# Performance work log

Hardware: AMD Instinct MI355X
Metric: run time of the kernel (lower is better)

Reference implementation:

```python
import jax, jax.numpy as jnp
import numpy as np

N_NODES = 50000
N_RAND_EDGES = 1_600_000
IN_FEATS = 512
HIDDEN = 256
NUM_CLASSES = 64


def setup_inputs() -> dict:
    key = jax.random.key(0)
    ks = jax.random.split(key, 6)
    src = jax.random.randint(ks[0], (N_RAND_EDGES,), 0, N_NODES, dtype=jnp.int32)
    dst = jax.random.randint(ks[1], (N_RAND_EDGES,), 0, N_NODES, dtype=jnp.int32)
    # dgl.add_self_loop(g): append (i, i) for every node
    loop = jnp.arange(N_NODES, dtype=jnp.int32)
    src = jnp.concatenate([src, loop])
    dst = jnp.concatenate([dst, loop])
    features = jax.random.normal(ks[2], (N_NODES, IN_FEATS), dtype=jnp.float32)
    W_conv = jax.random.normal(ks[3], (IN_FEATS, HIDDEN), dtype=jnp.float32) * (1.0 / np.sqrt(IN_FEATS))
    b_conv = jnp.zeros((HIDDEN,), dtype=jnp.float32)
    W2 = jax.random.normal(ks[4], (HIDDEN, NUM_CLASSES), dtype=jnp.float32) * (1.0 / np.sqrt(HIDDEN))
    b2 = jnp.zeros((NUM_CLASSES,), dtype=jnp.float32)
    return {"features": features, "W_conv": W_conv, "b_conv": b_conv,
            "W2": W2, "b2": b2, "src": src, "dst": dst}


def reference(features, W_conv, b_conv, W2, b2, src, dst):
    N = features.shape[0]
    ones = jnp.ones(src.shape[0], dtype=features.dtype)
    # symmetric ('both') normalization as in DGL GraphConv; self-loops guarantee deg >= 1
    deg_out = jax.ops.segment_sum(ones, src, num_segments=N)
    deg_in = jax.ops.segment_sum(ones, dst, num_segments=N)
    norm_src = jax.lax.rsqrt(deg_out)[:, None]  # [N, 1]
    norm_dst = jax.lax.rsqrt(deg_in)[:, None]
    # in_feats > hidden -> DGL multiplies by the weight before aggregating
    h = (features @ W_conv) * norm_src            # [N, H]
    agg = jax.ops.segment_sum(h[src], dst, num_segments=N)  # sparse SpMM: gather + scatter-add
    x = jax.nn.relu(agg * norm_dst + b_conv)      # [N, H]
    # dropout: identity in eval mode (deterministic reference)
    logits = x @ W2 + b2                          # [N, C]
    return jax.nn.log_softmax(logits, axis=1)
```

## Files before the change

### kernel.cpp

```cpp
#include <hip/hip_runtime.h>

typedef unsigned short u16;
typedef unsigned int u32;
typedef __attribute__((ext_vector_type(4))) float f32x4;
typedef __attribute__((ext_vector_type(8))) short s16x8;
typedef __attribute__((ext_vector_type(4))) unsigned short u16x4;
typedef __attribute__((ext_vector_type(8))) unsigned short u16x8;

#define IN_FEATS 512
#define HIDDEN   256
#define NCLS     64
#define NB       128
#define QBINS    12500
#define EPT      13

#define H8_CLIP  2.5f
#define H8_INV   (127.0f / H8_CLIP)
#define H8_SCALE (H8_CLIP / 127.0f)

static __device__ inline u16 f2bf(float f) {
    unsigned int u = __builtin_bit_cast(unsigned int, f);
    unsigned int r = (u + 0x7FFFu + ((u >> 16) & 1u)) >> 16;
    return (u16)r;
}
static __device__ inline float bf2f(u16 u) {
    unsigned int x = ((unsigned int)u) << 16;
    return __builtin_bit_cast(float, x);
}


__launch_bounds__(1024)
__global__ void khist(const int* __restrict__ src, const int* __restrict__ dst,
                      u32* __restrict__ P, int E, int N) {
    __shared__ int bins[QBINS];
    const int b = blockIdx.x;
    const int t = threadIdx.x;
    const int lo = (int)((long)b * E / NB);
    const int hi = (int)((long)(b + 1) * E / NB);

    int se[EPT], de[EPT];
#pragma unroll
    for (int p = 0; p < EPT; p++) {
        int e = lo + t + p * 1024;
        se[p] = 0; de[p] = 0;
        if (e < hi) { se[p] = src[e]; de[p] = dst[e]; }
    }

#pragma unroll 1
    for (int q = 0; q < 4; q++) {
        const int base = q * QBINS;
        __syncthreads();
        for (int j = t; j < QBINS; j += 1024) bins[j] = 0;
        __syncthreads();
#pragma unroll
        for (int p = 0; p < EPT; p++) {
            int e = lo + t + p * 1024;
            if (e < hi) {
                unsigned rs = (unsigned)(se[p] - base), rd = (unsigned)(de[p] - base);
                if (rs < (unsigned)QBINS) atomicAdd(&bins[rs], 1);
                if (rd < (unsigned)QBINS) atomicAdd(&bins[rd], 0x10000);
            }
        }
        for (int e = lo + t + EPT * 1024; e < hi; e += 1024) {
            int s = src[e], d = dst[e];
            unsigned rs = (unsigned)(s - base), rd = (unsigned)(d - base);
            if (rs < (unsigned)QBINS) atomicAdd(&bins[rs], 1);
            if (rd < (unsigned)QBINS) atomicAdd(&bins[rd], 0x10000);
        }
        __syncthreads();
        for (int j = t; j < QBINS; j += 1024) P[(size_t)b * 50000 + base + j] = (u32)bins[j];
    }
}

__global__ void kred(u32* __restrict__ P, int* __restrict__ deg_in,
                     float* __restrict__ ns, float* __restrict__ nd, int N) {
    int j = blockIdx.x * blockDim.x + threadIdx.x;
    if (j >= N) return;
    u32 so = 0, si = 0;
#pragma unroll 4
    for (int b = 0; b < NB; b++) {
        u32 v = P[(size_t)b * 50000 + j];
        P[(size_t)b * 50000 + j] = si;
        so += v & 0xffffu;
        si += v >> 16;
    }
    deg_in[j] = (int)si;
    ns[j] = rsqrtf((float)so);
    nd[j] = rsqrtf((float)si);
}

__launch_bounds__(256)
__global__ void kscanA(const int* __restrict__ deg, int* __restrict__ rowptr,
                       int* __restrict__ bsum, int N) {
    __shared__ int wsum[4];
    const int b = blockIdx.x, t = threadIdx.x;
    const int lane = t & 63, wave = t >> 6;
    const int j = b * 256 + t;
    int v = (j < N) ? deg[j] : 0;
    int s = v;
#pragma unroll
    for (int off = 1; off < 64; off <<= 1) {
        int u = __shfl_up(s, off);
        if (lane >= off) s += u;
    }
    if (lane == 63) wsum[wave] = s;
    __syncthreads();
    int woff = 0;
#pragma unroll
    for (int w = 0; w < 4; w++) woff += (w < wave) ? wsum[w] : 0;
    if (j < N) rowptr[j] = woff + s - v;
    if (t == 255) bsum[b] = woff + s;
}

__launch_bounds__(256)
__global__ void kscanB(int* __restrict__ rowptr, const int* __restrict__ bsum,
                       int N, int nblk, int E) {
    __shared__ int wsum[4];
    const int b = blockIdx.x, t = threadIdx.x;
    const int lane = t & 63, wave = t >> 6;
    int v = (t < b && t < nblk) ? bsum[t] : 0;
#pragma unroll
    for (int off = 32; off; off >>= 1) v += __shfl_xor(v, off);
    if (lane == 0) wsum[wave] = v;
    __syncthreads();
    int offsum = wsum[0] + wsum[1] + wsum[2] + wsum[3];
    int j = b * 256 + t;
    if (j < N) rowptr[j] += offsum;
    if (b == 0 && t == 0) rowptr[N] = E;
}

__launch_bounds__(1024)
__global__ void kscat(const int* __restrict__ src, const int* __restrict__ dst,
                      const int* __restrict__ rowptr, const u32* __restrict__ P,
                      int* __restrict__ csc, int E, int N) {
    __shared__ int cur[QBINS];
    const int b = blockIdx.x;
    const int t = threadIdx.x;
    const int lo = (int)((long)b * E / NB);
    const int hi = (int)((long)(b + 1) * E / NB);

    int se[EPT], de[EPT];
#pragma unroll
    for (int p = 0; p < EPT; p++) {
        int e = lo + t + p * 1024;
        se[p] = 0; de[p] = 0;
        if (e < hi) { se[p] = src[e]; de[p] = dst[e]; }
    }

#pragma unroll 1
    for (int q = 0; q < 4; q++) {
        const int base = q * QBINS;
        __syncthreads();
        for (int j = t; j < QBINS; j += 1024) {
            int node = base + j;
            cur[j] = (node < N) ? rowptr[node] + (int)P[(size_t)b * 50000 + node] : 0;
        }
        __syncthreads();
#pragma unroll
        for (int p = 0; p < EPT; p++) {
            int e = lo + t + p * 1024;
            if (e < hi) {
                unsigned rd = (unsigned)(de[p] - base);
                if (rd < (unsigned)QBINS) {
                    int pos = atomicAdd(&cur[rd], 1);
                    csc[pos] = se[p];
                }
            }
        }
        for (int e = lo + t + EPT * 1024; e < hi; e += 1024) {
            int d = dst[e];
            unsigned rd = (unsigned)(d - base);
            if (rd < (unsigned)QBINS) {
                int pos = atomicAdd(&cur[rd], 1);
                csc[pos] = src[e];
            }
        }
    }
}


__global__ void k_wt(const float* __restrict__ W, u16* __restrict__ Wt) {
    int i = blockIdx.x * blockDim.x + threadIdx.x;
    if (i < IN_FEATS * HIDDEN) {
        int k = i >> 8, n = i & 255;
        Wt[n * IN_FEATS + k] = f2bf(W[i]);
    }
}

__global__ void k_w2t(const float* __restrict__ W2, u16* __restrict__ W2t) {
    int i = blockIdx.x * blockDim.x + threadIdx.x;
    if (i < HIDDEN * NCLS) {
        int k = i >> 6, n = i & 63;
        W2t[n * HIDDEN + k] = f2bf(W2[i]);
    }
}


static __device__ inline s16x8 ld_frag(const u16* p) {
    u16x4 lo = *(const u16x4*)p;
    u16x4 hi = *(const u16x4*)(p + 4);
    s16x8 r;
    r[0] = (short)lo.x; r[1] = (short)lo.y; r[2] = (short)lo.z; r[3] = (short)lo.w;
    r[4] = (short)hi.x; r[5] = (short)hi.y; r[6] = (short)hi.z; r[7] = (short)hi.w;
    return r;
}

__launch_bounds__(512)
__global__ void k_gemm1(const float* __restrict__ feat, const u16* __restrict__ Wt,
                        const float* __restrict__ norm_src, signed char* __restrict__ h8, int N) {
    __shared__ __align__(16) u16 At[128][40];
    __shared__ __align__(16) u16 Bt[256][40];
    const int t = threadIdx.x;
    const int lane = t & 63;
    const int wave = t >> 6;
    const int wm = wave & 1;
    const int wn = wave >> 1;
    const int m0 = blockIdx.x * 128;
    const int l15 = lane & 15;
    const int l4 = lane >> 4;

    f32x4 acc[4][4] = {};

    for (int kk = 0; kk < IN_FEATS; kk += 32) {
        __syncthreads();
#pragma unroll
        for (int rnd = 0; rnd < 2; rnd++) {
            int slot = t + rnd * 512;
            int r = slot >> 3, q = slot & 7;
            int gr = m0 + r;
            float4 v = make_float4(0.f, 0.f, 0.f, 0.f);
            if (gr < N) v = *(const float4*)&feat[(size_t)gr * IN_FEATS + kk + q * 4];
            u16x4 p;
            p.x = f2bf(v.x); p.y = f2bf(v.y); p.z = f2bf(v.z); p.w = f2bf(v.w);
            *(u16x4*)&At[r][q * 4] = p;
        }
#pragma unroll
        for (int rnd = 0; rnd < 2; rnd++) {
            int slot = t + rnd * 512;
            int r = slot >> 2, q = slot & 3;
            u16x4 w0 = *(const u16x4*)&Wt[(size_t)r * IN_FEATS + kk + q * 8];
            u16x4 w1 = *(const u16x4*)&Wt[(size_t)r * IN_FEATS + kk + q * 8 + 4];
            *(u16x4*)&Bt[r][q * 8] = w0;
            *(u16x4*)&Bt[r][q * 8 + 4] = w1;
        }
        __syncthreads();

        s16x8 a[4], b[4];
#pragma unroll
        for (int mi = 0; mi < 4; mi++) a[mi] = ld_frag(&At[wm * 64 + mi * 16 + l15][l4 * 8]);
#pragma unroll
        for (int ni = 0; ni < 4; ni++) b[ni] = ld_frag(&Bt[wn * 64 + ni * 16 + l15][l4 * 8]);
#pragma unroll
        for (int mi = 0; mi < 4; mi++)
#pragma unroll
            for (int ni = 0; ni < 4; ni++)
                acc[mi][ni] = __builtin_amdgcn_mfma_f32_16x16x32_bf16(a[mi], b[ni], acc[mi][ni], 0, 0, 0);
    }

#pragma unroll
    for (int mi = 0; mi < 4; mi++) {
#pragma unroll
        for (int q = 0; q < 4; q++) {
            int row = m0 + wm * 64 + mi * 16 + l4 * 4 + q;
            if (row < N) {
                float nsv = norm_src[row] * H8_INV;
#pragma unroll
                for (int ni = 0; ni < 4; ni++) {
                    int col = wn * 64 + ni * 16 + l15;
                    int v = (int)rintf(acc[mi][ni][q] * nsv);
                    v = max(-127, min(127, v));
                    h8[(size_t)row * HIDDEN + col] = (signed char)v;
                }
            }
        }
    }
}

__global__ void k_spmm(const signed char* __restrict__ h8, const int* __restrict__ rowptr,
                       const int* __restrict__ csc, const float* __restrict__ nd,
                       const float* __restrict__ bconv, u16* __restrict__ x, int N) {
    const int lane = threadIdx.x & 63;
    const int gw = (blockIdx.x * blockDim.x + threadIdx.x) >> 6;
    const int nw = (gridDim.x * blockDim.x) >> 6;
    for (int node = gw; node < N; node += nw) {
        const int start = rowptr[node];
        const int end = rowptr[node + 1];
        int a0 = 0, a1 = 0, a2 = 0, a3 = 0;
        for (int base = start; base < end; base += 64) {
            int cnt = min(64, end - base);
            int ev = (lane < cnt) ? csc[base + lane] : 0;
            int i = 0;
            for (; i + 4 <= cnt; i += 4) {
                int s0 = __shfl(ev, i);
                int s1 = __shfl(ev, i + 1);
                int s2 = __shfl(ev, i + 2);
                int s3 = __shfl(ev, i + 3);
                int w0 = *(const int*)&h8[(size_t)s0 * HIDDEN + lane * 4];
                int w1 = *(const int*)&h8[(size_t)s1 * HIDDEN + lane * 4];
                int w2 = *(const int*)&h8[(size_t)s2 * HIDDEN + lane * 4];
                int w3 = *(const int*)&h8[(size_t)s3 * HIDDEN + lane * 4];
                a0 += ((w0 << 24) >> 24) + ((w1 << 24) >> 24) + ((w2 << 24) >> 24) + ((w3 << 24) >> 24);
                a1 += ((w0 << 16) >> 24) + ((w1 << 16) >> 24) + ((w2 << 16) >> 24) + ((w3 << 16) >> 24);
                a2 += ((w0 << 8) >> 24) + ((w1 << 8) >> 24) + ((w2 << 8) >> 24) + ((w3 << 8) >> 24);
                a3 += (w0 >> 24) + (w1 >> 24) + (w2 >> 24) + (w3 >> 24);
            }
            for (; i < cnt; i++) {
                int s = __shfl(ev, i);
                int w = *(const int*)&h8[(size_t)s * HIDDEN + lane * 4];
                a0 += (w << 24) >> 24;
                a1 += (w << 16) >> 24;
                a2 += (w << 8) >> 24;
                a3 += w >> 24;
            }
        }
        float scnd = nd[node] * H8_SCALE;
        int c0 = lane * 4;
        float b0 = bconv[c0], b1 = bconv[c0 + 1], b2v = bconv[c0 + 2], b3 = bconv[c0 + 3];
        u16x4 o;
        o.x = f2bf(fmaxf((float)a0 * scnd + b0, 0.f));
        o.y = f2bf(fmaxf((float)a1 * scnd + b1, 0.f));
        o.z = f2bf(fmaxf((float)a2 * scnd + b2v, 0.f));
        o.w = f2bf(fmaxf((float)a3 * scnd + b3, 0.f));
        *(u16x4*)&x[(size_t)node * HIDDEN + c0] = o;
    }
}

__launch_bounds__(256)
__global__ void k_gemm2(const u16* __restrict__ x, const u16* __restrict__ W2t,
                        const float* __restrict__ b2, float* __restrict__ out, int N) {
    __shared__ __align__(16) u16 Bs[NCLS][HIDDEN + 8];
    const int t = threadIdx.x;
    for (int i = t; i < NCLS * HIDDEN / 8; i += 256) {
        int idx = i * 8;
        int n = idx >> 8, k = idx & 255;
        *(u16x8*)&Bs[n][k] = *(const u16x8*)&W2t[n * HIDDEN + k];
    }
    __syncthreads();

    const int lane = t & 63;
    const int wave = t >> 6;
    const int l15 = lane & 15;
    const int l4 = lane >> 4;
    const int r0 = blockIdx.x * 128 + wave * 32;

    float bb[4];
#pragma unroll
    for (int ni = 0; ni < 4; ni++) bb[ni] = b2[ni * 16 + l15];

    f32x4 acc[2][4] = {};
#pragma unroll
    for (int kk = 0; kk < HIDDEN; kk += 32) {
        s16x8 b[4];
#pragma unroll
        for (int ni = 0; ni < 4; ni++) b[ni] = ld_frag(&Bs[ni * 16 + l15][kk + l4 * 8]);
#pragma unroll
        for (int mi = 0; mi < 2; mi++) {
            int row = r0 + mi * 16 + l15;
            s16x8 a = {};
            if (row < N) a = ld_frag(&x[(size_t)row * HIDDEN + kk + l4 * 8]);
#pragma unroll
            for (int ni = 0; ni < 4; ni++)
                acc[mi][ni] = __builtin_amdgcn_mfma_f32_16x16x32_bf16(a, b[ni], acc[mi][ni], 0, 0, 0);
        }
    }

#pragma unroll
    for (int mi = 0; mi < 2; mi++) {
#pragma unroll
        for (int q = 0; q < 4; q++) {
            int row = r0 + mi * 16 + l4 * 4 + q;
            float v0 = acc[mi][0][q] + bb[0];
            float v1 = acc[mi][1][q] + bb[1];
            float v2 = acc[mi][2][q] + bb[2];
            float v3 = acc[mi][3][q] + bb[3];
            float m = fmaxf(fmaxf(v0, v1), fmaxf(v2, v3));
#pragma unroll
            for (int off = 1; off < 16; off <<= 1) m = fmaxf(m, __shfl_xor(m, off));
            float s = __expf(v0 - m) + __expf(v1 - m) + __expf(v2 - m) + __expf(v3 - m);
#pragma unroll
            for (int off = 1; off < 16; off <<= 1) s += __shfl_xor(s, off);
            float lg = m + __logf(s);
            if (row < N) {
                out[(size_t)row * NCLS + 0 * 16 + l15] = v0 - lg;
                out[(size_t)row * NCLS + 1 * 16 + l15] = v1 - lg;
                out[(size_t)row * NCLS + 2 * 16 + l15] = v2 - lg;
                out[(size_t)row * NCLS + 3 * 16 + l15] = v3 - lg;
            }
        }
    }
}


extern "C" void kernel_launch(void* const* d_in, const int* in_sizes, int n_in,
                              void* d_out, int out_size, void* d_ws, size_t ws_size,
                              hipStream_t stream) {
    const float* feat = (const float*)d_in[0];
    const float* Wc   = (const float*)d_in[1];
    const float* bc   = (const float*)d_in[2];
    const float* W2   = (const float*)d_in[3];
    const float* b2   = (const float*)d_in[4];
    const int*   src  = (const int*)d_in[5];
    const int*   dst  = (const int*)d_in[6];
    const int N = in_sizes[0] / IN_FEATS;
    const int E = in_sizes[5];
    float* out = (float*)d_out;

    char* ws = (char*)d_ws;
    size_t off = 0;
    auto alloc = [&](size_t b) {
        char* p = ws + off;
        off = (off + b + 255) & ~(size_t)255;
        return p;
    };
    signed char* h8 = (signed char*)alloc((size_t)N * HIDDEN);
    u16* x      = (u16*)alloc((size_t)N * HIDDEN * 2);
    u16* Wt     = (u16*)alloc((size_t)IN_FEATS * HIDDEN * 2);
    u16* W2t    = (u16*)alloc((size_t)HIDDEN * NCLS * 2);
    int* deg_in = (int*)alloc((size_t)N * 4);
    int* rowptr = (int*)alloc((size_t)(N + 1) * 4);
    int* bsum   = (int*)alloc((size_t)256 * 4);
    float* ns   = (float*)alloc((size_t)N * 4);
    float* nd   = (float*)alloc((size_t)N * 4);
    int* csc    = (int*)alloc((size_t)E * 4);
    u32* P      = (u32*)alloc((size_t)NB * 50000 * 4);

    const int nblk = (N + 255) / 256;

    khist<<<dim3(NB), dim3(1024), 0, stream>>>(src, dst, P, E, N);
    kred<<<dim3((N + 255) / 256), dim3(256), 0, stream>>>(P, deg_in, ns, nd, N);
    kscanA<<<dim3(nblk), dim3(256), 0, stream>>>(deg_in, rowptr, bsum, N);
    kscanB<<<dim3(nblk), dim3(256), 0, stream>>>(rowptr, bsum, N, nblk, E);
    kscat<<<dim3(NB), dim3(1024), 0, stream>>>(src, dst, rowptr, P, csc, E, N);
    k_wt<<<dim3((IN_FEATS * HIDDEN + 255) / 256), dim3(256), 0, stream>>>(Wc, Wt);
    k_w2t<<<dim3((HIDDEN * NCLS + 255) / 256), dim3(256), 0, stream>>>(W2, W2t);
    k_gemm1<<<dim3((N + 127) / 128), dim3(512), 0, stream>>>(feat, Wt, ns, h8, N);
    k_spmm<<<dim3(2048), dim3(256), 0, stream>>>(h8, rowptr, csc, nd, bc, x, N);
    k_gemm2<<<dim3((N + 127) / 128), dim3(256), 0, stream>>>(x, W2t, b2, out, N);
}
```

Measured before the change: 175.5 us.

## Split SpMM waves across two nodes with 8-byte gathers and narrow histograms

The SpMM kernel now gives each half-wave its own destination node. Each lane gathers 8 int8 features per neighbor instead of 4, and the CSC entries are pre-scaled by 256 so they act directly as byte offsets into h8. Missing neighbors in the shorter of the two node lists point at an extra zero row appended to h8. The per-block histogram buffer P also shrinks from u32 to u16 by packing 8-bit out and in counts. That halves the histogram traffic, but it assumes no node gets more than 255 edges from a single block.

New measurement: 172.9 us. About the same (-1.5%).

```diff
diff --git a/kernel.cpp b/kernel.cpp
--- a/kernel.cpp
+++ b/kernel.cpp
@@ -31,7 +31,7 @@
 
 __launch_bounds__(1024)
 __global__ void khist(const int* __restrict__ src, const int* __restrict__ dst,
-                      u32* __restrict__ P, int E, int N) {
+                      u16* __restrict__ P, int E, int N) {
     __shared__ int bins[QBINS];
     const int b = blockIdx.x;
     const int t = threadIdx.x;
@@ -68,11 +68,14 @@
             if (rd < (unsigned)QBINS) atomicAdd(&bins[rd], 0x10000);
         }
         __syncthreads();
-        for (int j = t; j < QBINS; j += 1024) P[(size_t)b * 50000 + base + j] = (u32)bins[j];
-    }
-}
-
-__global__ void kred(u32* __restrict__ P, int* __restrict__ deg_in,
+        for (int j = t; j < QBINS; j += 1024) {
+            u32 v = (u32)bins[j];
+            P[(size_t)b * 50000 + base + j] = (u16)((v & 0xffu) | ((v >> 8) & 0xff00u));
+        }
+    }
+}
+
+__global__ void kred(u16* __restrict__ P, int* __restrict__ deg_in,
                      float* __restrict__ ns, float* __restrict__ nd, int N) {
     int j = blockIdx.x * blockDim.x + threadIdx.x;
     if (j >= N) return;
@@ -80,9 +83,9 @@
 #pragma unroll 4
     for (int b = 0; b < NB; b++) {
         u32 v = P[(size_t)b * 50000 + j];
-        P[(size_t)b * 50000 + j] = si;
-        so += v & 0xffffu;
-        si += v >> 16;
+        P[(size_t)b * 50000 + j] = (u16)si;
+        so += v & 0xffu;
+        si += v >> 8;
     }
     deg_in[j] = (int)si;
     ns[j] = rsqrtf((float)so);
@@ -131,7 +134,7 @@
 
 __launch_bounds__(1024)
 __global__ void kscat(const int* __restrict__ src, const int* __restrict__ dst,
-                      const int* __restrict__ rowptr, const u32* __restrict__ P,
+                      const int* __restrict__ rowptr, const u16* __restrict__ P,
                       int* __restrict__ csc, int E, int N) {
     __shared__ int cur[QBINS];
     const int b = blockIdx.x;
@@ -163,7 +166,7 @@
                 unsigned rd = (unsigned)(de[p] - base);
                 if (rd < (unsigned)QBINS) {
                     int pos = atomicAdd(&cur[rd], 1);
-                    csc[pos] = se[p];
+                    csc[pos] = se[p] << 8;
                 }
             }
         }
@@ -172,7 +175,7 @@
             unsigned rd = (unsigned)(d - base);
             if (rd < (unsigned)QBINS) {
                 int pos = atomicAdd(&cur[rd], 1);
-                csc[pos] = src[e];
+                csc[pos] = src[e] << 8;
             }
         }
     }
@@ -193,6 +196,10 @@
         int k = i >> 6, n = i & 63;
         W2t[n * HIDDEN + k] = f2bf(W2[i]);
     }
+}
+
+__global__ void k_zrow(signed char* __restrict__ h8, int N) {
+    ((int*)(h8 + (size_t)N * HIDDEN))[threadIdx.x] = 0;
 }
 
 
@@ -276,52 +283,80 @@
     }
 }
 
+__launch_bounds__(256)
 __global__ void k_spmm(const signed char* __restrict__ h8, const int* __restrict__ rowptr,
                        const int* __restrict__ csc, const float* __restrict__ nd,
                        const float* __restrict__ bconv, u16* __restrict__ x, int N) {
-    const int lane = threadIdx.x & 63;
-    const int gw = (blockIdx.x * blockDim.x + threadIdx.x) >> 6;
+    const int t = threadIdx.x;
+    const int lane = t & 63;
+    const int half = lane >> 5;
+    const int hl = lane & 31;
+    const int ZOFF = N * HIDDEN;
+    const int gw = (blockIdx.x * blockDim.x + t) >> 6;
     const int nw = (gridDim.x * blockDim.x) >> 6;
-    for (int node = gw; node < N; node += nw) {
-        const int start = rowptr[node];
-        const int end = rowptr[node + 1];
-        int a0 = 0, a1 = 0, a2 = 0, a3 = 0;
-        for (int base = start; base < end; base += 64) {
-            int cnt = min(64, end - base);
-            int ev = (lane < cnt) ? csc[base + lane] : 0;
+    const int npair = (N + 1) >> 1;
+
+    for (int pair = gw; pair < npair; pair += nw) {
+        int node = pair * 2 + half;
+        bool valid = node < N;
+        int start = 0, deg = 0;
+        if (valid) { start = rowptr[node]; deg = rowptr[node + 1] - start; }
+        int maxdeg = max(deg, __shfl_xor(deg, 32));
+        int a0 = 0, a1 = 0, a2 = 0, a3 = 0, a4 = 0, a5 = 0, a6 = 0, a7 = 0;
+
+        for (int base = 0; base < maxdeg; base += 32) {
+            int ev = ZOFF;
+            if (base + hl < deg) ev = csc[start + base + hl];
+            int cntmax = min(32, maxdeg - base);
             int i = 0;
-            for (; i + 4 <= cnt; i += 4) {
-                int s0 = __shfl(ev, i);
-                int s1 = __shfl(ev, i + 1);
-                int s2 = __shfl(ev, i + 2);
-                int s3 = __shfl(ev, i + 3);
-                int w0 = *(const int*)&h8[(size_t)s0 * HIDDEN + lane * 4];
-                int w1 = *(const int*)&h8[(size_t)s1 * HIDDEN + lane * 4];
-                int w2 = *(const int*)&h8[(size_t)s2 * HIDDEN + lane * 4];
-                int w3 = *(const int*)&h8[(size_t)s3 * HIDDEN + lane * 4];
-                a0 += ((w0 << 24) >> 24) + ((w1 << 24) >> 24) + ((w2 << 24) >> 24) + ((w3 << 24) >> 24);
-                a1 += ((w0 << 16) >> 24) + ((w1 << 16) >> 24) + ((w2 << 16) >> 24) + ((w3 << 16) >> 24);
-                a2 += ((w0 << 8) >> 24) + ((w1 << 8) >> 24) + ((w2 << 8) >> 24) + ((w3 << 8) >> 24);
-                a3 += (w0 >> 24) + (w1 >> 24) + (w2 >> 24) + (w3 >> 24);
-            }
-            for (; i < cnt; i++) {
-                int s = __shfl(ev, i);
-                int w = *(const int*)&h8[(size_t)s * HIDDEN + lane * 4];
-                a0 += (w << 24) >> 24;
-                a1 += (w << 16) >> 24;
-                a2 += (w << 8) >> 24;
-                a3 += w >> 24;
-            }
-        }
-        float scnd = nd[node] * H8_SCALE;
-        int c0 = lane * 4;
-        float b0 = bconv[c0], b1 = bconv[c0 + 1], b2v = bconv[c0 + 2], b3 = bconv[c0 + 3];
-        u16x4 o;
-        o.x = f2bf(fmaxf((float)a0 * scnd + b0, 0.f));
-        o.y = f2bf(fmaxf((float)a1 * scnd + b1, 0.f));
-        o.z = f2bf(fmaxf((float)a2 * scnd + b2v, 0.f));
-        o.w = f2bf(fmaxf((float)a3 * scnd + b3, 0.f));
-        *(u16x4*)&x[(size_t)node * HIDDEN + c0] = o;
+            for (; i + 4 <= cntmax; i += 4) {
+                int sb = (half << 5) + i;
+                int o0 = __shfl(ev, sb);
+                int o1 = __shfl(ev, sb + 1);
+                int o2 = __shfl(ev, sb + 2);
+                int o3 = __shfl(ev, sb + 3);
+                int2 w0 = *(const int2*)&h8[o0 + hl * 8];
+                int2 w1 = *(const int2*)&h8[o1 + hl * 8];
+                int2 w2 = *(const int2*)&h8[o2 + hl * 8];
+                int2 w3 = *(const int2*)&h8[o3 + hl * 8];
+                a0 += ((w0.x << 24) >> 24) + ((w1.x << 24) >> 24) + ((w2.x << 24) >> 24) + ((w3.x << 24) >> 24);
+                a1 += ((w0.x << 16) >> 24) + ((w1.x << 16) >> 24) + ((w2.x << 16) >> 24) + ((w3.x << 16) >> 24);
+                a2 += ((w0.x << 8) >> 24) + ((w1.x << 8) >> 24) + ((w2.x << 8) >> 24) + ((w3.x << 8) >> 24);
+                a3 += (w0.x >> 24) + (w1.x >> 24) + (w2.x >> 24) + (w3.x >> 24);
+                a4 += ((w0.y << 24) >> 24) + ((w1.y << 24) >> 24) + ((w2.y << 24) >> 24) + ((w3.y << 24) >> 24);
+                a5 += ((w0.y << 16) >> 24) + ((w1.y << 16) >> 24) + ((w2.y << 16) >> 24) + ((w3.y << 16) >> 24);
+                a6 += ((w0.y << 8) >> 24) + ((w1.y << 8) >> 24) + ((w2.y << 8) >> 24) + ((w3.y << 8) >> 24);
+                a7 += (w0.y >> 24) + (w1.y >> 24) + (w2.y >> 24) + (w3.y >> 24);
+            }
+            for (; i < cntmax; i++) {
+                int o = __shfl(ev, (half << 5) + i);
+                int2 w = *(const int2*)&h8[o + hl * 8];
+                a0 += (w.x << 24) >> 24;
+                a1 += (w.x << 16) >> 24;
+                a2 += (w.x << 8) >> 24;
+                a3 += w.x >> 24;
+                a4 += (w.y << 24) >> 24;
+                a5 += (w.y << 16) >> 24;
+                a6 += (w.y << 8) >> 24;
+                a7 += w.y >> 24;
+            }
+        }
+
+        if (valid) {
+            float scnd = nd[node] * H8_SCALE;
+            float4 ba = *(const float4*)&bconv[hl * 8];
+            float4 bb = *(const float4*)&bconv[hl * 8 + 4];
+            u16x8 o;
+            o[0] = f2bf(fmaxf((float)a0 * scnd + ba.x, 0.f));
+            o[1] = f2bf(fmaxf((float)a1 * scnd + ba.y, 0.f));
+            o[2] = f2bf(fmaxf((float)a2 * scnd + ba.z, 0.f));
+            o[3] = f2bf(fmaxf((float)a3 * scnd + ba.w, 0.f));
+            o[4] = f2bf(fmaxf((float)a4 * scnd + bb.x, 0.f));
+            o[5] = f2bf(fmaxf((float)a5 * scnd + bb.y, 0.f));
+            o[6] = f2bf(fmaxf((float)a6 * scnd + bb.z, 0.f));
+            o[7] = f2bf(fmaxf((float)a7 * scnd + bb.w, 0.f));
+            *(u16x8*)&x[(size_t)node * HIDDEN + hl * 8] = o;
+        }
     }
 }
 
@@ -412,7 +447,7 @@
         off = (off + b + 255) & ~(size_t)255;
         return p;
     };
-    signed char* h8 = (signed char*)alloc((size_t)N * HIDDEN);
+    signed char* h8 = (signed char*)alloc((size_t)(N + 1) * HIDDEN);
     u16* x      = (u16*)alloc((size_t)N * HIDDEN * 2);
     u16* Wt     = (u16*)alloc((size_t)IN_FEATS * HIDDEN * 2);
     u16* W2t    = (u16*)alloc((size_t)HIDDEN * NCLS * 2);
@@ -422,7 +457,7 @@
     float* ns   = (float*)alloc((size_t)N * 4);
     float* nd   = (float*)alloc((size_t)N * 4);
     int* csc    = (int*)alloc((size_t)E * 4);
-    u32* P      = (u32*)alloc((size_t)NB * 50000 * 4);
+    u16* P      = (u16*)alloc((size_t)NB * 50000 * 2);
 
     const int nblk = (N + 255) / 256;
 
@@ -433,6 +468,7 @@
     kscat<<<dim3(NB), dim3(1024), 0, stream>>>(src, dst, rowptr, P, csc, E, N);
     k_wt<<<dim3((IN_FEATS * HIDDEN + 255) / 256), dim3(256), 0, stream>>>(Wc, Wt);
     k_w2t<<<dim3((HIDDEN * NCLS + 255) / 256), dim3(256), 0, stream>>>(W2, W2t);
+    k_zrow<<<dim3(1), dim3(64), 0, stream>>>(h8, N);
     k_gemm1<<<dim3((N + 127) / 128), dim3(512), 0, stream>>>(feat, Wt, ns, h8, N);
     k_spmm<<<dim3(2048), dim3(256), 0, stream>>>(h8, rowptr, csc, nd, bc, x, N);
     k_gemm2<<<dim3((N + 127) / 128), dim3(256), 0, stream>>>(x, W2t, b2, out, N);
```
